# Performance work log

Hardware: AMD Instinct MI355X
Metric: run time of the kernel (lower is better)

Reference implementation:

```python
import jax, jax.numpy as jnp
import numpy as np

H = 16  # headNum
D = 1024  # d_model
DK = D // H


def setup_inputs() -> dict:
    key = jax.random.key(0)
    ks = jax.random.split(key, 11)
    B, S = 2, 2048
    scale = 1.0 / np.sqrt(D)
    inp = {
        'query': jax.random.normal(ks[0], (B, S, D), jnp.float32),
        'key':   jax.random.normal(ks[1], (B, S, D), jnp.float32),
        'value': jax.random.normal(ks[2], (B, S, D), jnp.float32),
        # nn.Linear params: W is [out, in], y = x @ W.T + b
        'Wq': jax.random.normal(ks[3], (D, D), jnp.float32) * scale,
        'bq': jnp.zeros((D,), jnp.float32),
        'Wk': jax.random.normal(ks[4], (D, D), jnp.float32) * scale,
        'bk': jnp.zeros((D,), jnp.float32),
        'Wv': jax.random.normal(ks[5], (D, D), jnp.float32) * scale,
        'bv': jnp.zeros((D,), jnp.float32),
        'Wo': jax.random.normal(ks[6], (D, D), jnp.float32) * scale,
        'bo': jnp.zeros((D,), jnp.float32),
    }
    return inp


def reference(query, key, value, Wq, bq, Wk, bk, Wv, bv, Wo, bo):
    B, S, _ = query.shape
    # projections (torch Linear: x @ W.T + b), split heads -> [B, H, S, DK]
    q = (query @ Wq.T + bq).reshape(B, S, H, DK).transpose(0, 2, 1, 3)
    k = (key   @ Wk.T + bk).reshape(B, S, H, DK).transpose(0, 2, 1, 3)
    v = (value @ Wv.T + bv).reshape(B, S, H, DK).transpose(0, 2, 1, 3)
    # scores [B, H, S, S] = Q K^T / sqrt(d_k)  (fully materialized, as in source)
    scores = jnp.einsum('bhqd,bhkd->bhqk', q, k) * (DK ** -0.5)
    p_attn = jax.nn.softmax(scores, axis=-1)  # dropout = identity (eval)
    x = jnp.einsum('bhqk,bhkd->bhqd', p_attn, v)
    x = x.transpose(0, 2, 1, 3).reshape(B, S, H * DK)
    return x @ Wo.T + bo
```

## Files before the change

kernel.cpp:

```cpp
#include <hip/hip_runtime.h>

#define BATCH 2
#define SEQ   2048
#define NH    16
#define DK    64
#define DM    1024
#define MROWS 4096
#define NX    4194304
#define NW    1048576

typedef __attribute__((ext_vector_type(8))) short bf16x8;
typedef __attribute__((ext_vector_type(4))) short bf16x4;
typedef __attribute__((ext_vector_type(4))) float f32x4;
typedef __attribute__((ext_vector_type(4))) unsigned short us16x4;
typedef __attribute__((ext_vector_type(2))) unsigned int u32x2;

#if __has_builtin(__builtin_amdgcn_mfma_f32_16x16x16bf16_1k)
#define MFMA16(a, b, c) __builtin_amdgcn_mfma_f32_16x16x16bf16_1k(a, b, c, 0, 0, 0)
#else
#define MFMA16(a, b, c) (c)
#endif

__device__ __forceinline__ unsigned short f2bf(float f) {
  unsigned int u = __builtin_bit_cast(unsigned int, f);
  u += 0x7FFFu + ((u >> 16) & 1u);
  return (unsigned short)(u >> 16);
}

__device__ __forceinline__ unsigned int pkbf(float hi, float lo) {
#if __has_builtin(__builtin_amdgcn_perm)
  return __builtin_amdgcn_perm(__builtin_bit_cast(unsigned int, hi),
                               __builtin_bit_cast(unsigned int, lo), 0x07060302u);
#else
  return (__builtin_bit_cast(unsigned int, hi) & 0xffff0000u) |
         (__builtin_bit_cast(unsigned int, lo) >> 16);
#endif
}

__device__ __forceinline__ void g2l16(void* lds, const void* g) {
  __builtin_amdgcn_global_load_lds(
      (const __attribute__((address_space(1))) void*)g,
      (__attribute__((address_space(3))) void*)lds, 16, 0, 0);
}

__global__ __launch_bounds__(256) void cast_all(
    const float* __restrict__ q, const float* __restrict__ k, const float* __restrict__ v,
    const float* __restrict__ wq, const float* __restrict__ wk,
    const float* __restrict__ wv, const float* __restrict__ wo,
    unsigned short* __restrict__ dst) {
  size_t e = ((size_t)blockIdx.x * 256 + threadIdx.x) * 4;
  const float* src;
  if      (e < (size_t)NX)        src = q  + e;
  else if (e < (size_t)2*NX)      src = k  + (e - (size_t)NX);
  else if (e < (size_t)3*NX)      src = v  + (e - (size_t)2*NX);
  else if (e < (size_t)3*NX+NW)   src = wq + (e - (size_t)3*NX);
  else if (e < (size_t)3*NX+2*NW) src = wk + (e - (size_t)3*NX-NW);
  else if (e < (size_t)3*NX+3*NW) src = wv + (e - (size_t)3*NX-2*NW);
  else                            src = wo + (e - (size_t)3*NX-3*NW);
  float4 f = *(const float4*)src;
  us16x4 o;
  o[0] = f2bf(f.x); o[1] = f2bf(f.y); o[2] = f2bf(f.z); o[3] = f2bf(f.w);
  *(us16x4*)(dst + e) = o;
}

template <int MODE, int BM>
__global__ __launch_bounds__(256) void gemm_bt(
    const unsigned short* __restrict__ Xbase, const unsigned short* __restrict__ Wbase,
    const float* __restrict__ b0, const float* __restrict__ b1, const float* __restrict__ b2,
    unsigned short* __restrict__ qkv_dst, float* __restrict__ fout, float qscale) {
  constexpr int IM = BM / 32;
  constexpr int ASHOTS = (BM * 32) / 2048;
  const int tid  = threadIdx.x;
  const int lane = tid & 63;
  const int w    = tid >> 6;
  const int wm   = w >> 1, wn = w & 1;
  const int x15  = lane & 15, quad = lane >> 4;
  const int row0 = blockIdx.x * BM;
  const int col0 = blockIdx.y * 128;
  const int z    = blockIdx.z;

  const unsigned short* A  = Xbase + (size_t)z * NX;
  const unsigned short* Wp = Wbase + (size_t)z * NW;
  const float* bias = (MODE == 0) ? (z == 0 ? b0 : (z == 1 ? b1 : b2)) : b0;
  const float zs = (MODE == 0 && z == 0) ? qscale : 1.0f;

  __shared__ __align__(16) unsigned short At[2][BM * 32];
  __shared__ __align__(16) unsigned short Bt[2][128 * 32];

  f32x4 acc[IM][4] = {};

  auto stage = [&](int buf, int kt) {
#pragma unroll
    for (int j = 0; j < ASHOTS; ++j) {
      int e = (j * 256 + tid) * 8;
      int r = e >> 5, c = e & 31;
      g2l16(&At[buf][e], A + (size_t)(row0 + r) * DM + kt + c);
    }
#pragma unroll
    for (int j = 0; j < 2; ++j) {
      int e = (j * 256 + tid) * 8;
      int r = e >> 5, c = e & 31;
      g2l16(&Bt[buf][e], Wp + (size_t)(col0 + r) * DM + kt + c);
    }
  };

  stage(0, 0);
  for (int it = 0; it < DM / 32; ++it) {
    const int cur = it & 1;
    __syncthreads();
    if (it + 1 < DM / 32) stage(cur ^ 1, (it + 1) * 32);
    bf16x8 af[IM], bfv[4];
#pragma unroll
    for (int i = 0; i < IM; ++i)
      af[i] = *(const bf16x8*)&At[cur][(wm * (BM / 2) + i * 16 + x15) * 32 + quad * 8];
#pragma unroll
    for (int jn = 0; jn < 4; ++jn)
      bfv[jn] = *(const bf16x8*)&Bt[cur][(wn * 64 + jn * 16 + x15) * 32 + quad * 8];
#pragma unroll
    for (int i = 0; i < IM; ++i)
#pragma unroll
      for (int jn = 0; jn < 4; ++jn)
        acc[i][jn] = __builtin_amdgcn_mfma_f32_16x16x32_bf16(af[i], bfv[jn], acc[i][jn], 0, 0, 0);
  }

#pragma unroll
  for (int jn = 0; jn < 4; ++jn) {
    const int n = col0 + wn * 64 + jn * 16 + x15;
    const float bv = bias[n];
#pragma unroll
    for (int i = 0; i < IM; ++i) {
      const int m0 = row0 + wm * (BM / 2) + i * 16 + quad * 4;
      if (MODE == 0 && z == 2) {
        us16x4 pk;
#pragma unroll
        for (int r = 0; r < 4; ++r) pk[r] = f2bf(acc[i][jn][r] + bv);
        const int b = m0 >> 11, s = m0 & 2047;
        const int h = n >> 6,  dk = n & 63;
        *(us16x4*)&qkv_dst[(size_t)2 * NX + (((size_t)(b * NH + h) * DK + dk) << 11) + s] = pk;
      } else {
#pragma unroll
        for (int r = 0; r < 4; ++r) {
          const int m = m0 + r;
          float val = (acc[i][jn][r] + bv) * zs;
          if (MODE == 0) {
            const int b = m >> 11, s = m & 2047;
            const int h = n >> 6,  dk = n & 63;
            qkv_dst[(size_t)z * NX + (((size_t)(b * NH + h) * SEQ + s) << 6) + dk] = f2bf(val);
          } else {
            fout[(size_t)m * DM + n] = val;
          }
        }
      }
    }
  }
}

__global__ __launch_bounds__(256, 2) void attn(
    const unsigned short* __restrict__ Qb, const unsigned short* __restrict__ Kb,
    const unsigned short* __restrict__ VTb, unsigned short* __restrict__ AO) {
  const int tid  = threadIdx.x;
  const int lane = tid & 63;
  const int w    = tid >> 6;
  const int wq   = w & 1;
  const int ws   = w >> 1;
  const int x15  = lane & 15, quad = lane >> 4;
  const int lin = (int)(blockIdx.x | (blockIdx.y << 4) | (blockIdx.z << 8));
  const int swz = ((lin & 7) << 6) | (lin >> 3);
  const int qt = swz & 15;
  const int h  = (swz >> 4) & 15;
  const int b  = swz >> 8;
  const size_t bh = ((size_t)(b * NH + h)) * SEQ * DK;
  const unsigned short* Q  = Qb  + bh;
  const unsigned short* K  = Kb  + bh;
  const unsigned short* VT = VTb + bh;
  const int q0 = qt * 128;

  __shared__ __align__(16) unsigned char smem[2 * 64 * 68 * 4];
  unsigned short* Kl = (unsigned short*)smem;
  unsigned short* Vl = (unsigned short*)(smem + 16384);
  float* Ored = (float*)smem;
  __shared__ float lbuf[2][4][128];

  bf16x8 qf[4][2];
#pragma unroll
  for (int qgi = 0; qgi < 4; ++qgi)
#pragma unroll
    for (int ks = 0; ks < 2; ++ks)
      qf[qgi][ks] = *(const bf16x8*)&Q[(size_t)(q0 + wq * 64 + qgi * 16 + x15) * DK + ks * 32 + quad * 8];

  f32x4 po[4][4] = {};
  float pol[4] = {0.f, 0.f, 0.f, 0.f};

  const int sK0 = tid >> 3,          sK1 = (tid + 256) >> 3;
  const int dgK0 = (tid & 7) ^ (sK0 & 7), dgK1 = (tid & 7) ^ (sK1 & 7);

  auto stageKV = [&](int buf, int s0) {
    g2l16(&Kl[buf * 4096 + tid * 8],         K + (size_t)(s0 + sK0) * DK + dgK0 * 8);
    g2l16(&Kl[buf * 4096 + (tid + 256) * 8], K + (size_t)(s0 + sK1) * DK + dgK1 * 8);
    g2l16(&Vl[buf * 4096 + tid * 8],         VT + (size_t)sK0 * SEQ + s0 + dgK0 * 8);
    g2l16(&Vl[buf * 4096 + (tid + 256) * 8], VT + (size_t)sK1 * SEQ + s0 + dgK1 * 8);
  };

  stageKV(0, 0);
  for (int s0 = 0; s0 < SEQ; s0 += 64) {
    const int cur = (s0 >> 6) & 1;
    __syncthreads();
    if (s0 + 64 < SEQ) stageKV(cur ^ 1, s0 + 64);

    bf16x8 kf[2][2];
#pragma unroll
    for (int shi = 0; shi < 2; ++shi) {
      const int sh = ws * 2 + shi;
      const int kbase = (sh * 16 + x15) * 8;
      kf[shi][0] = *(const bf16x8*)&Kl[cur * 4096 + (kbase + ((0 + quad) ^ (x15 & 7))) * 8];
      kf[shi][1] = *(const bf16x8*)&Kl[cur * 4096 + (kbase + ((4 + quad) ^ (x15 & 7))) * 8];
    }
    bf16x4 vf[2][4];
#pragma unroll
    for (int shi = 0; shi < 2; ++shi)
#pragma unroll
      for (int nt = 0; nt < 4; ++nt) {
        const int d = nt * 16 + x15;
        const int sg = ((ws * 2 + shi) * 2 + (quad >> 1)) ^ (d & 7);
        vf[shi][nt] = *(const bf16x4*)&Vl[cur * 4096 + (d * 8 + sg) * 8 + (quad & 1) * 4];
      }

    __builtin_amdgcn_s_setprio(1);
#pragma unroll
    for (int shi = 0; shi < 2; ++shi) {
#pragma unroll
      for (int qgi = 0; qgi < 4; ++qgi) {
        f32x4 sacc = {};
        sacc = __builtin_amdgcn_mfma_f32_16x16x32_bf16(kf[shi][0], qf[qgi][0], sacc, 0, 0, 0);
        sacc = __builtin_amdgcn_mfma_f32_16x16x32_bf16(kf[shi][1], qf[qgi][1], sacc, 0, 0, 0);
        float p0 = __builtin_amdgcn_exp2f(sacc[0]);
        float p1 = __builtin_amdgcn_exp2f(sacc[1]);
        float p2 = __builtin_amdgcn_exp2f(sacc[2]);
        float p3 = __builtin_amdgcn_exp2f(sacc[3]);
        pol[qgi] += (p0 + p1) + (p2 + p3);
        u32x2 uu;
        uu[0] = pkbf(p1, p0);
        uu[1] = pkbf(p3, p2);
        bf16x4 pf = __builtin_bit_cast(bf16x4, uu);
#pragma unroll
        for (int nt = 0; nt < 4; ++nt)
          po[qgi][nt] = MFMA16(vf[shi][nt], pf, po[qgi][nt]);
      }
    }
    __builtin_amdgcn_s_setprio(0);
  }

#pragma unroll
  for (int qgi = 0; qgi < 4; ++qgi)
    lbuf[ws][quad][wq * 64 + qgi * 16 + x15] = pol[qgi];
  __syncthreads();

  const int qq = tid >> 2;
  const int d0 = (tid & 3) * 16;
#pragma unroll
  for (int rw = 0; rw < 2; ++rw) {
    if (wq == rw) {
#pragma unroll
      for (int qgi = 0; qgi < 4; ++qgi)
#pragma unroll
        for (int nt = 0; nt < 4; ++nt)
          *(f32x4*)&Ored[(ws * 64 + qgi * 16 + x15) * 68 + nt * 16 + quad * 4] = po[qgi][nt];
    }
    __syncthreads();
    float ls = 0.f;
#pragma unroll
    for (int w2 = 0; w2 < 2; ++w2)
#pragma unroll
      for (int qd = 0; qd < 4; ++qd)
        ls += lbuf[w2][qd][rw * 64 + qq];
    const float inv = 1.0f / ls;
    const size_t orow = ((size_t)(b * SEQ + q0 + rw * 64 + qq)) * DM + h * DK + d0;
#pragma unroll
    for (int c = 0; c < 4; ++c) {
      f32x4 sa = *(const f32x4*)&Ored[(0 * 64 + qq) * 68 + d0 + c * 4];
      f32x4 sb = *(const f32x4*)&Ored[(1 * 64 + qq) * 68 + d0 + c * 4];
      us16x4 pk;
#pragma unroll
      for (int r = 0; r < 4; ++r) pk[r] = f2bf((sa[r] + sb[r]) * inv);
      *(us16x4*)&AO[orow + c * 4] = pk;
    }
    __syncthreads();
  }
}

extern "C" void kernel_launch(void* const* d_in, const int* in_sizes, int n_in,
                              void* d_out, int out_size, void* d_ws, size_t ws_size,
                              hipStream_t stream) {
  const float* q  = (const float*)d_in[0];
  const float* k  = (const float*)d_in[1];
  const float* v  = (const float*)d_in[2];
  const float* wq = (const float*)d_in[3];
  const float* bq = (const float*)d_in[4];
  const float* wk = (const float*)d_in[5];
  const float* bk = (const float*)d_in[6];
  const float* wv = (const float*)d_in[7];
  const float* bv = (const float*)d_in[8];
  const float* wo = (const float*)d_in[9];
  const float* bo = (const float*)d_in[10];
  float* out = (float*)d_out;

  unsigned short* ws = (unsigned short*)d_ws;
  unsigned short* Xq = ws;
  unsigned short* Wb = ws + (size_t)3 * NX;
  unsigned short* Qb = ws + (size_t)3 * NX + 4 * NW;
  unsigned short* AO = Qb + (size_t)3 * NX;

  const float qscale = 0.125f * 1.4426950408889634f;

  cast_all<<<16384, 256, 0, stream>>>(q, k, v, wq, wk, wv, wo, ws);
  gemm_bt<0, 128><<<dim3(32, 8, 3), 256, 0, stream>>>(Xq, Wb, bq, bk, bv, Qb, nullptr, qscale);
  attn<<<dim3(16, 16, 2), 256, 0, stream>>>(Qb, Qb + (size_t)NX, Qb + (size_t)2 * NX, AO);
  gemm_bt<1, 64><<<dim3(64, 8, 1), 256, 0, stream>>>(AO, Wb + (size_t)3 * NW, bo, bo, bo,
                                                     nullptr, out, 1.0f);
}
```

Baseline: 220.0 us.

## Triple-buffer GEMM and attention LDS staging with vmcnt-based waits

Both the projection GEMM and the attention kernel move from double to triple buffering in LDS. Each iteration waits with an explicit s_waitcnt vmcnt on the older loads and then a raw s_barrier, instead of a full __syncthreads. This keeps two tiles of global-to-LDS loads in flight to hide memory latency. It costs more LDS, which can lower occupancy, and it issues redundant wrapped-around loads on the last iterations; the attention loop also drops the setprio hints.

Result: slower. 232.0 us (+5.4%).

```diff
diff --git a/kernel.cpp b/kernel.cpp
--- a/kernel.cpp
+++ b/kernel.cpp
@@ -84,8 +84,8 @@
   const float* bias = (MODE == 0) ? (z == 0 ? b0 : (z == 1 ? b1 : b2)) : b0;
   const float zs = (MODE == 0 && z == 0) ? qscale : 1.0f;
 
-  __shared__ __align__(16) unsigned short At[2][BM * 32];
-  __shared__ __align__(16) unsigned short Bt[2][128 * 32];
+  __shared__ __align__(16) unsigned short At[3][BM * 32];
+  __shared__ __align__(16) unsigned short Bt[3][128 * 32];
 
   f32x4 acc[IM][4] = {};
 
@@ -104,24 +104,30 @@
     }
   };
 
+  int ca = 0, cb = 1, cc = 2;
   stage(0, 0);
+  stage(1, 32);
   for (int it = 0; it < DM / 32; ++it) {
-    const int cur = it & 1;
-    __syncthreads();
-    if (it + 1 < DM / 32) stage(cur ^ 1, (it + 1) * 32);
+    if constexpr (ASHOTS + 2 == 4) asm volatile("s_waitcnt vmcnt(4)" ::: "memory");
+    else                           asm volatile("s_waitcnt vmcnt(3)" ::: "memory");
+    __builtin_amdgcn_sched_barrier(0);
+    __builtin_amdgcn_s_barrier();
+    stage(cc, ((it + 2) * 32) & (DM - 1));
     bf16x8 af[IM], bfv[4];
 #pragma unroll
     for (int i = 0; i < IM; ++i)
-      af[i] = *(const bf16x8*)&At[cur][(wm * (BM / 2) + i * 16 + x15) * 32 + quad * 8];
+      af[i] = *(const bf16x8*)&At[ca][(wm * (BM / 2) + i * 16 + x15) * 32 + quad * 8];
 #pragma unroll
     for (int jn = 0; jn < 4; ++jn)
-      bfv[jn] = *(const bf16x8*)&Bt[cur][(wn * 64 + jn * 16 + x15) * 32 + quad * 8];
+      bfv[jn] = *(const bf16x8*)&Bt[ca][(wn * 64 + jn * 16 + x15) * 32 + quad * 8];
 #pragma unroll
     for (int i = 0; i < IM; ++i)
 #pragma unroll
       for (int jn = 0; jn < 4; ++jn)
         acc[i][jn] = __builtin_amdgcn_mfma_f32_16x16x32_bf16(af[i], bfv[jn], acc[i][jn], 0, 0, 0);
+    int t = ca; ca = cb; cb = cc; cc = t;
   }
+  asm volatile("s_waitcnt vmcnt(0)" ::: "memory");
 
 #pragma unroll
   for (int jn = 0; jn < 4; ++jn) {
@@ -175,9 +181,9 @@
   const unsigned short* VT = VTb + bh;
   const int q0 = qt * 128;
 
-  __shared__ __align__(16) unsigned char smem[2 * 64 * 68 * 4];
-  unsigned short* Kl = (unsigned short*)smem;
-  unsigned short* Vl = (unsigned short*)(smem + 16384);
+  __shared__ __align__(16) unsigned short smem[3 * 4096 * 2];
+  unsigned short* Kl = smem;
+  unsigned short* Vl = smem + 12288;
   float* Ored = (float*)smem;
   __shared__ float lbuf[2][4][128];
 
@@ -195,25 +201,30 @@
   const int dgK0 = (tid & 7) ^ (sK0 & 7), dgK1 = (tid & 7) ^ (sK1 & 7);
 
   auto stageKV = [&](int buf, int s0) {
-    g2l16(&Kl[buf * 4096 + tid * 8],         K + (size_t)(s0 + sK0) * DK + dgK0 * 8);
-    g2l16(&Kl[buf * 4096 + (tid + 256) * 8], K + (size_t)(s0 + sK1) * DK + dgK1 * 8);
-    g2l16(&Vl[buf * 4096 + tid * 8],         VT + (size_t)sK0 * SEQ + s0 + dgK0 * 8);
-    g2l16(&Vl[buf * 4096 + (tid + 256) * 8], VT + (size_t)sK1 * SEQ + s0 + dgK1 * 8);
+    const int bo = buf * 4096;
+    g2l16(&Kl[bo + tid * 8],         K + (size_t)(s0 + sK0) * DK + dgK0 * 8);
+    g2l16(&Kl[bo + (tid + 256) * 8], K + (size_t)(s0 + sK1) * DK + dgK1 * 8);
+    g2l16(&Vl[bo + tid * 8],         VT + (size_t)sK0 * SEQ + s0 + dgK0 * 8);
+    g2l16(&Vl[bo + (tid + 256) * 8], VT + (size_t)sK1 * SEQ + s0 + dgK1 * 8);
   };
 
+  int ca = 0, cb = 1, cc = 2;
   stageKV(0, 0);
-  for (int s0 = 0; s0 < SEQ; s0 += 64) {
-    const int cur = (s0 >> 6) & 1;
-    __syncthreads();
-    if (s0 + 64 < SEQ) stageKV(cur ^ 1, s0 + 64);
+  stageKV(1, 64);
+  for (int i = 0; i < SEQ / 64; ++i) {
+    asm volatile("s_waitcnt vmcnt(4)" ::: "memory");
+    __builtin_amdgcn_sched_barrier(0);
+    __builtin_amdgcn_s_barrier();
+    stageKV(cc, ((i + 2) * 64) & (SEQ - 1));
+    const int ko = ca * 4096;
 
     bf16x8 kf[2][2];
 #pragma unroll
     for (int shi = 0; shi < 2; ++shi) {
       const int sh = ws * 2 + shi;
       const int kbase = (sh * 16 + x15) * 8;
-      kf[shi][0] = *(const bf16x8*)&Kl[cur * 4096 + (kbase + ((0 + quad) ^ (x15 & 7))) * 8];
-      kf[shi][1] = *(const bf16x8*)&Kl[cur * 4096 + (kbase + ((4 + quad) ^ (x15 & 7))) * 8];
+      kf[shi][0] = *(const bf16x8*)&Kl[ko + (kbase + ((0 + quad) ^ (x15 & 7))) * 8];
+      kf[shi][1] = *(const bf16x8*)&Kl[ko + (kbase + ((4 + quad) ^ (x15 & 7))) * 8];
     }
     bf16x4 vf[2][4];
 #pragma unroll
@@ -222,10 +233,9 @@
       for (int nt = 0; nt < 4; ++nt) {
         const int d = nt * 16 + x15;
         const int sg = ((ws * 2 + shi) * 2 + (quad >> 1)) ^ (d & 7);
-        vf[shi][nt] = *(const bf16x4*)&Vl[cur * 4096 + (d * 8 + sg) * 8 + (quad & 1) * 4];
+        vf[shi][nt] = *(const bf16x4*)&Vl[ko + (d * 8 + sg) * 8 + (quad & 1) * 4];
       }
 
-    __builtin_amdgcn_s_setprio(1);
 #pragma unroll
     for (int shi = 0; shi < 2; ++shi) {
 #pragma unroll
@@ -247,7 +257,7 @@
           po[qgi][nt] = MFMA16(vf[shi][nt], pf, po[qgi][nt]);
       }
     }
-    __builtin_amdgcn_s_setprio(0);
+    int t = ca; ca = cb; cb = cc; cc = t;
   }
 
 #pragma unroll
```
